# Optimization experiments

Measured on AMD Instinct MI355X. Metric: run time of the kernel, lower is better.

The kernel has to match this reference:

```python
import jax, jax.numpy as jnp
import numpy as np

# ---- static config (matches init_kwargs) ----
CANVAS = (18, 24, 24)
TILE = (6, 8, 8)
KERNEL = (1, 3, 3)
TEXT_LEN = 320
B, H, D = 1, 4, 128
SCALE = 1.0 / np.sqrt(D)

TT, TH, TW = TILE
NT, NH, NW = CANVAS[0] // TT, CANVAS[1] // TH, CANVAS[2] // TW
BLOCK = TT * TH * TW                      # 384
N_IMG = NT * NH * NW                      # 27 image blocks
IMG_LEN = CANVAS[0] * CANVAS[1] * CANVAS[2]
TEXT_BLOCKS = -(-TEXT_LEN // BLOCK)       # 1
TEXT_PAD = TEXT_BLOCKS * BLOCK - TEXT_LEN # 64
TOTAL_BLOCKS = N_IMG + TEXT_BLOCKS        # 28
SEQ_LEN = IMG_LEN + TEXT_LEN


def _sta_kv_blocks():
    """Per-image-block allowed KV block indices (incl. text blocks), [N_IMG, n_allowed]."""
    kt, kh, kw = KERNEL
    idx = np.arange(N_IMG)
    qt = idx // (NH * NW)
    qh = (idx % (NH * NW)) // NW
    qw = idx % NW
    ct = np.clip(qt, kt // 2, NT - 1 - kt // 2)
    ch = np.clip(qh, kh // 2, NH - 1 - kh // 2)
    cw = np.clip(qw, kw // 2, NW - 1 - kw // 2)
    mask = ((np.abs(ct[:, None] - qt[None, :]) <= kt // 2)
            & (np.abs(ch[:, None] - qh[None, :]) <= kh // 2)
            & (np.abs(cw[:, None] - qw[None, :]) <= kw // 2))
    text_ids = np.arange(N_IMG, TOTAL_BLOCKS)
    rows = [np.concatenate([np.nonzero(mask[i])[0], text_ids]) for i in range(N_IMG)]
    return np.stack(rows)  # uniform n_allowed by clamping

KV_BLOCKS = jnp.asarray(_sta_kv_blocks())  # [N_IMG, NA]
NA = KV_BLOCKS.shape[1]                    # 10


def _tile(x):
    # [B,H,IMG_LEN,D] raster -> tile order
    x = x.reshape(B, H, NT, TT, NH, TH, NW, TW, D)
    x = x.transpose(0, 1, 2, 4, 6, 3, 5, 7, 8)
    return x.reshape(B, H, N_IMG * BLOCK, D)


def _untile(x):
    x = x.reshape(B, H, NT, NH, NW, TT, TH, TW, D)
    x = x.transpose(0, 1, 2, 5, 3, 6, 4, 7, 8)
    return x.reshape(B, H, IMG_LEN, D)


def _prep(x):
    # split image/text, tile image, zero-pad text to block multiple, concat
    img = _tile(x[:, :, :IMG_LEN])
    txt = jnp.pad(x[:, :, IMG_LEN:], ((0, 0), (0, 0), (0, TEXT_PAD), (0, 0)))
    return jnp.concatenate([img, txt], axis=2)  # [B,H,TOTAL_BLOCKS*BLOCK,D]


def setup_inputs() -> dict:
    key = jax.random.key(0)
    kq, kk, kv = jax.random.split(key, 3)
    shape = (B, H, SEQ_LEN, D)
    return {
        "q": jax.random.normal(kq, shape, dtype=jnp.float32),
        "k": jax.random.normal(kk, shape, dtype=jnp.float32),
        "v": jax.random.normal(kv, shape, dtype=jnp.float32),
    }


def reference(q, k, v):
    Q, K, V = _prep(q), _prep(k), _prep(v)
    Qb = Q.reshape(B, H, TOTAL_BLOCKS, BLOCK, D)
    Kb = K.reshape(B, H, TOTAL_BLOCKS, BLOCK, D)
    Vb = V.reshape(B, H, TOTAL_BLOCKS, BLOCK, D)

    # ---- image blocks: grouped block-sparse attention (KV gathered per block) ----
    Qi = Qb[:, :, :N_IMG]                                   # [B,H,N_IMG,BLOCK,D]
    Ki = Kb[:, :, KV_BLOCKS].reshape(B, H, N_IMG, NA * BLOCK, D)
    Vi = Vb[:, :, KV_BLOCKS].reshape(B, H, N_IMG, NA * BLOCK, D)
    s = jnp.einsum("bhnqd,bhnkd->bhnqk", Qi, Ki) * SCALE
    p = jax.nn.softmax(s, axis=-1)
    oi = jnp.einsum("bhnqk,bhnkd->bhnqd", p, Vi)            # [B,H,N_IMG,BLOCK,D]

    # ---- text blocks: dense attention over full (tiled img + padded text) KV ----
    Qt = Qb[:, :, N_IMG:].reshape(B, H, TEXT_BLOCKS * BLOCK, D)
    st = jnp.einsum("bhqd,bhkd->bhqk", Qt, K) * SCALE
    ot = jnp.einsum("bhqk,bhkd->bhqd", jax.nn.softmax(st, axis=-1), V)

    img_out = _untile(oi.reshape(B, H, N_IMG * BLOCK, D))
    return jnp.concatenate([img_out, ot[:, :, :TEXT_LEN]], axis=2)  # [B,H,SEQ_LEN,D]
```

## Files before the change

kernel.cpp:

```cpp
#include <hip/hip_runtime.h>

#define SEQ      10688
#define IMG_LEN  10368
#define TEXT_LEN 320
#define DH       128
#define NHEADS   4
#define SLAB     3456
#define KVC      32
#define QT       128
#define NIT      81
#define NTT      3
#define NCH_TXT  334
#define NCH_IMG  118
#define SCALEL2E 0.12751744518924593f
#define DEFER_THR 8.0f

typedef __bf16 bf16x8 __attribute__((ext_vector_type(8)));
typedef __bf16 bf16x4 __attribute__((ext_vector_type(4)));
typedef float  f32x4  __attribute__((ext_vector_type(4)));

__device__ __forceinline__ unsigned pk2bf(float a, float b) {
    union { __bf16 h[2]; unsigned u; } t;
    t.h[0] = (__bf16)a; t.h[1] = (__bf16)b;
    return t.u;
}

__device__ __forceinline__ float fexp2(float x) {
    float r;
    asm("v_exp_f32 %0, %1" : "=v"(r) : "v"(x));
    return r;
}
__device__ __forceinline__ unsigned cvtpk(float a, float b) {
    unsigned r;
    asm("v_cvt_pk_bf16_f32 %0, %1, %2" : "=v"(r) : "v"(a), "v"(b));
    return r;
}

__device__ __forceinline__ bf16x8 as_bf16x8(uint4 u) {
    union { uint4 a; bf16x8 v; } t; t.a = u; return t.v;
}

__device__ __forceinline__ void split_range(int total, int nsplit, int s, int& c0, int& n) {
    const int q = total / nsplit, r = total % nsplit;
    if (s < r) { c0 = s * (q + 1); n = q + 1; }
    else       { c0 = r * (q + 1) + (s - r) * q; n = q; }
}

template<int TS, int IS> struct Geo {
    static constexpr int NTXTB = NHEADS * NTT * TS;
    static constexpr int NIMGB = NHEADS * NIT * IS;
    static constexpr int NPID  = NTXTB + NIMGB;
    static constexpr size_t WS_FLOATS = (size_t)NPID * (QT * DH + QT * 2);
};
#define KB_BYTES ((size_t)NHEADS * SEQ * DH * 2)

__global__ __launch_bounds__(256) void sta_prep(const float* __restrict__ Kg,
                                                const float* __restrict__ Vg,
                                                uint4* __restrict__ Kf,
                                                uint4* __restrict__ Vf) {
    __shared__ float T[64][65];
    const int b = blockIdx.x;
    if (b < NHEADS * 334) {
        const int hb = b / 334, chunk = b % 334;
        const float* src = Kg + ((size_t)hb * SEQ + chunk * 32) * DH;
        const int t = threadIdx.x;
        #pragma unroll
        for (int i = 0; i < 2; ++i) {
            const int oidx = t + 256 * i;
            const int frag = oidx >> 6, lane = oidx & 63;
            const int c = frag >> 1, kt = frag & 1;
            const int row = kt * 16 + (lane & 15);
            const int col = c * 32 + (lane >> 4) * 8;
            float4 a = *(const float4*)(src + (size_t)row * DH + col);
            float4 d = *(const float4*)(src + (size_t)row * DH + col + 4);
            uint4 u; u.x = pk2bf(a.x, a.y); u.y = pk2bf(a.z, a.w);
                     u.z = pk2bf(d.x, d.y); u.w = pk2bf(d.z, d.w);
            Kf[((size_t)(hb * 334 + chunk) * 8 + frag) * 64 + lane] = u;
        }
    } else {
        const int bb = b - NHEADS * 334;
        const int dhalf = bb & 1, kvt = (bb >> 1) % 167, h = (bb >> 1) / 167;
        const float* src = Vg + ((size_t)h * SEQ + kvt * 64) * DH + dhalf * 64;
        const int t = threadIdx.x;
        const int col = t & 63, r4 = t >> 6;
        #pragma unroll
        for (int i = 0; i < 16; ++i) {
            const int row = i * 4 + r4;
            T[row][col] = src[(size_t)row * DH + col];
        }
        __syncthreads();
        const int lane = t & 63, q = t & 15, gg = lane >> 4;
        #pragma unroll
        for (int i = 0; i < 2; ++i) {
            const int idx = (t >> 6) * 2 + i;
            const int ch2 = idx >> 2, kt = (idx >> 1) & 1, dtp = idx & 1;
            const int kvl = ch2 * 32 + kt * 16 + gg * 4;
            const int dle = dtp * 32 + q;
            const int dlo = dle + 16;
            uint4 u;
            u.x = pk2bf(T[kvl][dle],     T[kvl + 1][dle]);
            u.y = pk2bf(T[kvl + 2][dle], T[kvl + 3][dle]);
            u.z = pk2bf(T[kvl][dlo],     T[kvl + 1][dlo]);
            u.w = pk2bf(T[kvl + 2][dlo], T[kvl + 3][dlo]);
            const size_t o4 = ((size_t)(h * 334 + kvt * 2 + ch2) * 8
                               + kt * 4 + dhalf * 2 + dtp) * 64 + lane;
            Vf[o4] = u;
        }
    }
}

template<int TS, int IS, bool SPLIT>
__global__ __launch_bounds__(256) void sta_attn(const float* __restrict__ Qg,
                                                const uint4* __restrict__ Kf,
                                                const uint4* __restrict__ Vf,
                                                float* __restrict__ Og,
                                                float* __restrict__ Opart,
                                                float* __restrict__ Ml) {
    using G = Geo<TS, IS>;
    const int tid  = threadIdx.x;
    const int lane = tid & 63;
    const int wv   = tid >> 6;
    const int q    = lane & 15;
    const int g    = lane >> 4;

    int b = blockIdx.x;
    int head, qbase, nch, ch0, kvb0, pid = 0;
    bool isText;
    if (b < G::NTXTB) {
        int tb = b / TS, s = b % TS;
        head = tb / NTT; qbase = IMG_LEN + (tb % NTT) * QT;
        isText = true; kvb0 = 0;
        split_range(NCH_TXT, TS, s, ch0, nch);
        pid = b;
    } else {
        int bb = b - G::NTXTB; int tile = bb / IS, s = bb % IS;
        head = tile / NIT; qbase = (tile % NIT) * QT;
        isText = false; kvb0 = (qbase / SLAB) * SLAB;
        split_range(NCH_IMG, IS, s, ch0, nch);
        pid = G::NTXTB + bb;
    }

    const size_t hoff = (size_t)head * SEQ * DH;
    const float* Qh = Qg + hoff;
    const uint4* kfh = Kf + (size_t)head * 334 * 512 + lane;
    const uint4* vfh = Vf + (size_t)head * 334 * 512 + lane;

    bf16x8 qf[2][4];
    #pragma unroll
    for (int n = 0; n < 2; ++n) {
        int qr = qbase + wv * 32 + n * 16 + q;
        if (qr > SEQ - 1) qr = SEQ - 1;
        const float* qp = Qh + (size_t)qr * DH;
        #pragma unroll
        for (int c = 0; c < 4; ++c) {
            float4 a = *(const float4*)(qp + c * 32 + g * 8);
            float4 d = *(const float4*)(qp + c * 32 + g * 8 + 4);
            union { unsigned u[4]; bf16x8 v; } t;
            t.u[0] = pk2bf(a.x * SCALEL2E, a.y * SCALEL2E);
            t.u[1] = pk2bf(a.z * SCALEL2E, a.w * SCALEL2E);
            t.u[2] = pk2bf(d.x * SCALEL2E, d.y * SCALEL2E);
            t.u[3] = pk2bf(d.z * SCALEL2E, d.w * SCALEL2E);
            qf[n][c] = t.v;
        }
    }

    f32x4 o[2][8];
    #pragma unroll
    for (int n = 0; n < 2; ++n)
        #pragma unroll
        for (int dt = 0; dt < 8; ++dt) o[n][dt] = f32x4{0.f, 0.f, 0.f, 0.f};
    float mrun[2] = {-INFINITY, -INFINITY};
    float lsum[2] = {0.f, 0.f};

    auto kvaddr = [&](int gch) -> int {
        return isText ? gch * KVC
                      : (gch < 108 ? kvb0 + gch * KVC : IMG_LEN + (gch - 108) * KVC);
    };

    uint4 kf4[8];
    {
        const uint4* kp = kfh + (size_t)(kvaddr(ch0) >> 5) * 512;
        #pragma unroll
        for (int f = 0; f < 8; ++f) kf4[f] = kp[f * 64];
    }

    for (int ch = 0; ch < nch; ++ch) {
        const int kb = kvaddr(ch0 + ch);

        const uint4* vp = vfh + (size_t)(kb >> 5) * 512;
        uint4 vf4[8];
        #pragma unroll
        for (int f = 0; f < 8; ++f) vf4[f] = vp[f * 64];

        f32x4 st[2][2];
        #pragma unroll
        for (int n = 0; n < 2; ++n)
            #pragma unroll
            for (int kt = 0; kt < 2; ++kt) st[n][kt] = f32x4{0.f, 0.f, 0.f, 0.f};
        __builtin_amdgcn_s_setprio(1);
        #pragma unroll
        for (int c = 0; c < 4; ++c) {
            #pragma unroll
            for (int kt = 0; kt < 2; ++kt) {
                bf16x8 kf = as_bf16x8(kf4[c * 2 + kt]);
                st[0][kt] = __builtin_amdgcn_mfma_f32_16x16x32_bf16(kf, qf[0][c], st[0][kt], 0, 0, 0);
                st[1][kt] = __builtin_amdgcn_mfma_f32_16x16x32_bf16(kf, qf[1][c], st[1][kt], 0, 0, 0);
            }
        }
        __builtin_amdgcn_s_setprio(0);

        float cm[2];
        #pragma unroll
        for (int n = 0; n < 2; ++n) {
            float a0 = fmaxf(fmaxf(st[n][0][0], st[n][0][1]), st[n][0][2]);
            float a1 = fmaxf(fmaxf(st[n][0][3], st[n][1][0]), st[n][1][1]);
            float a2 = fmaxf(fmaxf(st[n][1][2], st[n][1][3]), a0);
            float c0 = fmaxf(a1, a2);
            c0 = fmaxf(c0, __shfl_xor(c0, 16));
            c0 = fmaxf(c0, __shfl_xor(c0, 32));
            cm[n] = c0;
        }
        if (!__all((cm[0] <= mrun[0] + DEFER_THR) && (cm[1] <= mrun[1] + DEFER_THR))) {
            #pragma unroll
            for (int n = 0; n < 2; ++n) {
                float mnew = fmaxf(mrun[n], cm[n]);
                float sc = fexp2(mrun[n] - mnew);
                lsum[n] *= sc;
                mrun[n] = mnew;
                f32x4 scv;
                #pragma unroll
                for (int r = 0; r < 4; ++r)
                    scv[r] = __shfl(sc, (lane & 48) + g * 4 + r);
                #pragma unroll
                for (int dt = 0; dt < 8; ++dt) o[n][dt] *= scv;
            }
        }

        bf16x4 pkv[2][2];
        #pragma unroll
        for (int n = 0; n < 2; ++n) {
            float ps = 0.f;
            #pragma unroll
            for (int kt = 0; kt < 2; ++kt) {
                float p0 = fexp2(st[n][kt][0] - mrun[n]);
                float p1 = fexp2(st[n][kt][1] - mrun[n]);
                float p2 = fexp2(st[n][kt][2] - mrun[n]);
                float p3 = fexp2(st[n][kt][3] - mrun[n]);
                ps += (p0 + p1) + (p2 + p3);
                union { unsigned u[2]; bf16x4 v; } t;
                t.u[0] = cvtpk(p0, p1);
                t.u[1] = cvtpk(p2, p3);
                pkv[n][kt] = t.v;
            }
            lsum[n] += ps;
        }

        if (ch + 1 < nch) {
            const uint4* kp = kfh + (size_t)(kvaddr(ch0 + ch + 1) >> 5) * 512;
            #pragma unroll
            for (int f = 0; f < 8; ++f) kf4[f] = kp[f * 64];
        }

        __builtin_amdgcn_s_setprio(1);
        #pragma unroll
        for (int kt = 0; kt < 2; ++kt) {
            #pragma unroll
            for (int dt = 0; dt < 8; ++dt) {
                bf16x4 vb = ((const bf16x4*)&vf4[kt * 4 + (dt >> 1)])[dt & 1];
                asm("v_mfma_f32_16x16x16_bf16 %0, %1, %2, %0"
                    : "+v"(o[0][dt]) : "v"(pkv[0][kt]), "v"(vb));
                asm("v_mfma_f32_16x16x16_bf16 %0, %1, %2, %0"
                    : "+v"(o[1][dt]) : "v"(pkv[1][kt]), "v"(vb));
            }
        }
        __builtin_amdgcn_s_setprio(0);
    }

    asm volatile("s_nop 7\n\ts_nop 7");

    #pragma unroll
    for (int n = 0; n < 2; ++n) {
        lsum[n] += __shfl_xor(lsum[n], 16);
        lsum[n] += __shfl_xor(lsum[n], 32);
    }

    if constexpr (SPLIT) {
        float* opb = Opart + (size_t)pid * (QT * DH);
        #pragma unroll
        for (int n = 0; n < 2; ++n) {
            #pragma unroll
            for (int r = 0; r < 4; ++r) {
                const int row = wv * 32 + n * 16 + g * 4 + r;
                float* op = opb + row * DH + q;
                #pragma unroll
                for (int dt = 0; dt < 8; ++dt) op[dt * 16] = o[n][dt][r];
            }
            if (g == 0) {
                const int srow = wv * 32 + n * 16 + q;
                Ml[(size_t)pid * (QT * 2) + srow * 2]     = mrun[n];
                Ml[(size_t)pid * (QT * 2) + srow * 2 + 1] = lsum[n];
            }
        }
    } else {
        #pragma unroll
        for (int n = 0; n < 2; ++n) {
            const float inv = 1.f / (lsum[n] + 64.f * fexp2(-mrun[n]));
            f32x4 invv;
            #pragma unroll
            for (int r = 0; r < 4; ++r)
                invv[r] = __shfl(inv, (lane & 48) + g * 4 + r);
            #pragma unroll
            for (int r = 0; r < 4; ++r) {
                const int qrow = qbase + wv * 32 + n * 16 + g * 4 + r;
                if (qrow >= SEQ) continue;
                float* op = Og + hoff + (size_t)qrow * DH + q;
                #pragma unroll
                for (int dt = 0; dt < 8; ++dt) op[dt * 16] = o[n][dt][r] * invv[r];
            }
        }
    }
}

template<int S>
__device__ __forceinline__ void merge_body(const float* __restrict__ Opart,
                                           const float* __restrict__ Ml,
                                           float* __restrict__ Og,
                                           int head, int qbase, int pbase,
                                           int row, int c4) {
    if (qbase + row >= SEQ) return;
    float w[S], lv[S];
    float m = -INFINITY;
    #pragma unroll
    for (int s = 0; s < S; ++s) {
        w[s]  = Ml[(size_t)(pbase + s) * (QT * 2) + row * 2];
        lv[s] = Ml[(size_t)(pbase + s) * (QT * 2) + row * 2 + 1];
        m = fmaxf(m, w[s]);
    }
    float L = 64.f * exp2f(-m);
    #pragma unroll
    for (int s = 0; s < S; ++s) { w[s] = exp2f(w[s] - m); L += w[s] * lv[s]; }
    const float inv = 1.f / L;

    float* op = Og + (size_t)head * SEQ * DH + (size_t)(qbase + row) * DH;
    #pragma unroll
    for (int half = 0; half < 2; ++half) {
        const int j = c4 + half * 16;
        float4 acc = make_float4(0.f, 0.f, 0.f, 0.f);
        #pragma unroll
        for (int s = 0; s < S; ++s) {
            const float4 p = *(const float4*)(Opart + (size_t)(pbase + s) * (QT * DH)
                                              + row * DH + j * 4);
            acc.x += w[s] * p.x; acc.y += w[s] * p.y;
            acc.z += w[s] * p.z; acc.w += w[s] * p.w;
        }
        float4 v; v.x = acc.x * inv; v.y = acc.y * inv; v.z = acc.z * inv; v.w = acc.w * inv;
        *(float4*)(op + j * 4) = v;
    }
}

template<int TS, int IS>
__global__ __launch_bounds__(256) void sta_merge(const float* __restrict__ Opart,
                                                 const float* __restrict__ Ml,
                                                 float* __restrict__ Og) {
    const int bb = blockIdx.x;
    const int b = bb >> 3, slice = bb & 7;
    const int t = threadIdx.x;
    const int row = slice * 16 + (t >> 4);
    const int c4  = t & 15;
    if (b < NHEADS * NTT) {
        merge_body<TS>(Opart, Ml, Og, b / NTT, IMG_LEN + (b % NTT) * QT,
                       b * TS, row, c4);
    } else {
        const int tile = b - NHEADS * NTT;
        merge_body<IS>(Opart, Ml, Og, tile / NIT, (tile % NIT) * QT,
                       NHEADS * NTT * TS + tile * IS, row, c4);
    }
}

extern "C" void kernel_launch(void* const* d_in, const int* in_sizes, int n_in,
                              void* d_out, int out_size, void* d_ws, size_t ws_size,
                              hipStream_t stream) {
    const float* Qg = (const float*)d_in[0];
    const float* Kg = (const float*)d_in[1];
    const float* Vg = (const float*)d_in[2];
    float* Og = (float*)d_out;
    char* wsb = (char*)d_ws;

    uint4* Kfb = (uint4*)wsb;
    uint4* Vfb = (uint4*)(wsb + KB_BYTES);
    float* Opart = (float*)(wsb + 2 * KB_BYTES);
    const int nprep  = NHEADS * 334 + NHEADS * 2 * 167;
    const int nmerge = NHEADS * (NTT + NIT) * 8;

    if (ws_size >= 2 * KB_BYTES + Geo<8, 4>::WS_FLOATS * sizeof(float)) {
        float* Ml = Opart + (size_t)Geo<8, 4>::NPID * QT * DH;
        hipLaunchKernelGGL(sta_prep, dim3(nprep), dim3(256), 0, stream, Kg, Vg, Kfb, Vfb);
        hipLaunchKernelGGL((sta_attn<8, 4, true>), dim3(Geo<8, 4>::NPID), dim3(256), 0, stream,
                           Qg, Kfb, Vfb, Og, Opart, Ml);
        hipLaunchKernelGGL((sta_merge<8, 4>), dim3(nmerge), dim3(256), 0, stream,
                           Opart, Ml, Og);
    } else if (ws_size >= 2 * KB_BYTES + Geo<4, 2>::WS_FLOATS * sizeof(float)) {
        float* Ml = Opart + (size_t)Geo<4, 2>::NPID * QT * DH;
        hipLaunchKernelGGL(sta_prep, dim3(nprep), dim3(256), 0, stream, Kg, Vg, Kfb, Vfb);
        hipLaunchKernelGGL((sta_attn<4, 2, true>), dim3(Geo<4, 2>::NPID), dim3(256), 0, stream,
                           Qg, Kfb, Vfb, Og, Opart, Ml);
        hipLaunchKernelGGL((sta_merge<4, 2>), dim3(nmerge), dim3(256), 0, stream,
                           Opart, Ml, Og);
    } else {
        hipLaunchKernelGGL(sta_prep, dim3(nprep), dim3(256), 0, stream, Kg, Vg, Kfb, Vfb);
        hipLaunchKernelGGL((sta_attn<1, 1, false>), dim3(Geo<1, 1>::NPID), dim3(256), 0, stream,
                           Qg, Kfb, Vfb, Og, (float*)nullptr, (float*)nullptr);
    }
}
```

Measured before the change: 155.6 us.

## Use 16x16x32 bf16 MFMA for PV product with repacked V fragments

Changes the P·V step from pairs of 16x16x16 bf16 MFMAs to single 16x16x32 bf16 MFMAs by packing both k-halves of P into one 8-wide bf16 vector. The V prep kernel is rewritten to lay out fragments so each lane holds 8 contiguous k-values per d-tile. This halves the MFMA instruction count for the PV product and drops the inline-asm MFMAs and trailing nop padding. The risk is that the new layout must match the MFMA operand mapping exactly.

```diff
diff --git a/kernel.cpp b/kernel.cpp
--- a/kernel.cpp
+++ b/kernel.cpp
@@ -16,7 +16,6 @@
 #define DEFER_THR 8.0f
 
 typedef __bf16 bf16x8 __attribute__((ext_vector_type(8)));
-typedef __bf16 bf16x4 __attribute__((ext_vector_type(4)));
 typedef float  f32x4  __attribute__((ext_vector_type(4)));
 
 __device__ __forceinline__ unsigned pk2bf(float a, float b) {
@@ -89,21 +88,21 @@
             T[row][col] = src[(size_t)row * DH + col];
         }
         __syncthreads();
-        const int lane = t & 63, q = t & 15, gg = lane >> 4;
+        const int lane = t & 63, dq = t & 15, gg = lane >> 4;
         #pragma unroll
         for (int i = 0; i < 2; ++i) {
             const int idx = (t >> 6) * 2 + i;
-            const int ch2 = idx >> 2, kt = (idx >> 1) & 1, dtp = idx & 1;
-            const int kvl = ch2 * 32 + kt * 16 + gg * 4;
-            const int dle = dtp * 32 + q;
-            const int dlo = dle + 16;
+            const int ch2 = idx >> 2, dtl = idx & 3;
+            const int kvb = ch2 * 32 + gg * 4;
+            const int d = dtl * 16 + dq;
             uint4 u;
-            u.x = pk2bf(T[kvl][dle],     T[kvl + 1][dle]);
-            u.y = pk2bf(T[kvl + 2][dle], T[kvl + 3][dle]);
-            u.z = pk2bf(T[kvl][dlo],     T[kvl + 1][dlo]);
-            u.w = pk2bf(T[kvl + 2][dlo], T[kvl + 3][dlo]);
+            u.x = pk2bf(T[kvb + 0][d],      T[kvb + 1][d]);
+            u.y = pk2bf(T[kvb + 2][d],      T[kvb + 3][d]);
+            u.z = pk2bf(T[kvb + 16][d],     T[kvb + 17][d]);
+            u.w = pk2bf(T[kvb + 18][d],     T[kvb + 19][d]);
+            const int dtglob = dhalf * 4 + dtl;
             const size_t o4 = ((size_t)(h * 334 + kvt * 2 + ch2) * 8
-                               + kt * 4 + dhalf * 2 + dtp) * 64 + lane;
+                               + dtglob) * 64 + lane;
             Vf[o4] = u;
         }
     }
@@ -236,10 +235,11 @@
             }
         }
 
-        bf16x4 pkv[2][2];
+        bf16x8 pa[2];
         #pragma unroll
         for (int n = 0; n < 2; ++n) {
             float ps = 0.f;
+            union { unsigned u[4]; bf16x8 v; } t;
             #pragma unroll
             for (int kt = 0; kt < 2; ++kt) {
                 float p0 = fexp2(st[n][kt][0] - mrun[n]);
@@ -247,11 +247,10 @@
                 float p2 = fexp2(st[n][kt][2] - mrun[n]);
                 float p3 = fexp2(st[n][kt][3] - mrun[n]);
                 ps += (p0 + p1) + (p2 + p3);
-                union { unsigned u[2]; bf16x4 v; } t;
-                t.u[0] = cvtpk(p0, p1);
-                t.u[1] = cvtpk(p2, p3);
-                pkv[n][kt] = t.v;
-            }
+                t.u[kt * 2]     = cvtpk(p0, p1);
+                t.u[kt * 2 + 1] = cvtpk(p2, p3);
+            }
+            pa[n] = t.v;
             lsum[n] += ps;
         }
 
@@ -263,20 +262,13 @@
 
         __builtin_amdgcn_s_setprio(1);
         #pragma unroll
-        for (int kt = 0; kt < 2; ++kt) {
-            #pragma unroll
-            for (int dt = 0; dt < 8; ++dt) {
-                bf16x4 vb = ((const bf16x4*)&vf4[kt * 4 + (dt >> 1)])[dt & 1];
-                asm("v_mfma_f32_16x16x16_bf16 %0, %1, %2, %0"
-                    : "+v"(o[0][dt]) : "v"(pkv[0][kt]), "v"(vb));
-                asm("v_mfma_f32_16x16x16_bf16 %0, %1, %2, %0"
-                    : "+v"(o[1][dt]) : "v"(pkv[1][kt]), "v"(vb));
-            }
+        for (int dt = 0; dt < 8; ++dt) {
+            bf16x8 vb = as_bf16x8(vf4[dt]);
+            o[0][dt] = __builtin_amdgcn_mfma_f32_16x16x32_bf16(pa[0], vb, o[0][dt], 0, 0, 0);
+            o[1][dt] = __builtin_amdgcn_mfma_f32_16x16x32_bf16(pa[1], vb, o[1][dt], 0, 0, 0);
         }
         __builtin_amdgcn_s_setprio(0);
     }
-
-    asm volatile("s_nop 7\n\ts_nop 7");
 
     #pragma unroll
     for (int n = 0; n < 2; ++n) {
```

Result: slower. 196.4 us (+26.2%).
